# Optimization experiments

Hardware: AMD Instinct MI355X
Metric: run time of the kernel (lower is better)

The kernel has to match this reference:

```python
import jax, jax.numpy as jnp
import numpy as np

EPS = 1e-5
LOCAL_WINDOW = 256
NUM_HEADS = 16


def _layernorm(x, g, b):
    m = jnp.mean(x, axis=-1, keepdims=True)
    v = jnp.mean(jnp.square(x - m), axis=-1, keepdims=True)
    return (x - m) * jax.lax.rsqrt(v + EPS) * g + b


def _rotate_half(x):
    x1, x2 = jnp.split(x, 2, axis=-1)
    return jnp.concatenate([-x2, x1], axis=-1)


def _rope_cos_sin(s, d, base=10000.0):
    half = d // 2
    inv_freq = 1.0 / base ** (jnp.arange(half, dtype=jnp.float32) / float(half))
    t = jnp.arange(s, dtype=jnp.float32)
    freqs = jnp.einsum('s,d->sd', t, inv_freq)          # [s, half]
    emb = jnp.concatenate([freqs, freqs], axis=-1)       # [s, d]
    return jnp.cos(emb)[None, None, :, :], jnp.sin(emb)[None, None, :, :]


def setup_inputs() -> dict:
    key = jax.random.key(0)
    ks = jax.random.split(key, 8)
    B, S, D, F = 2, 2048, 1024, 4096
    sc = lambda d: 1.0 / np.sqrt(d)
    return {
        'x': jax.random.normal(ks[0], (B, S, D), jnp.float32),
        'w_qkv': jax.random.normal(ks[1], (D, 3 * D), jnp.float32) * sc(D),
        'w_out': jax.random.normal(ks[2], (D, D), jnp.float32) * sc(D),
        'g1': jnp.ones((D,), jnp.float32),
        'b1': jnp.zeros((D,), jnp.float32),
        'g2': jnp.ones((D,), jnp.float32),
        'b2': jnp.zeros((D,), jnp.float32),
        'w_gate': jax.random.normal(ks[3], (D, F), jnp.float32) * sc(D),
        'b_gate': jnp.zeros((F,), jnp.float32),
        'w_up': jax.random.normal(ks[4], (D, F), jnp.float32) * sc(D),
        'b_up': jnp.zeros((F,), jnp.float32),
        'w_down': jax.random.normal(ks[5], (F, D), jnp.float32) * sc(F),
        'b_down': jnp.zeros((D,), jnp.float32),
    }


def reference(x, w_qkv, w_out, g1, b1, g2, b2, w_gate, b_gate, w_up, b_up, w_down, b_down):
    B, S, D = x.shape
    H = NUM_HEADS
    hd = D // H

    # ---- pre-norm + RoPE self-attention ----
    y = _layernorm(x, g1, b1)
    qkv = jnp.einsum('bsd,de->bse', y, w_qkv)
    q, k, v = jnp.split(qkv, 3, axis=-1)
    split_heads = lambda t: t.reshape(B, S, H, hd).transpose(0, 2, 1, 3)  # [b,h,s,hd]
    q, k, v = split_heads(q), split_heads(k), split_heads(v)

    cos, sin = _rope_cos_sin(S, hd)
    q = q * cos + _rotate_half(q) * sin
    k = k * cos + _rotate_half(k) * sin

    scale = float(hd) ** -0.5
    logits = jnp.einsum('bhid,bhjd->bhij', q, k) * scale

    i = jnp.arange(S)[:, None]
    j = jnp.arange(S)[None, :]
    can = (jnp.abs(j - i) <= LOCAL_WINDOW) & (j <= i)    # local + causal band
    logits = jnp.where(can[None, None], logits, jnp.float32(-1e9))

    attn = jax.nn.softmax(logits, axis=-1)
    o = jnp.einsum('bhij,bhjd->bhid', attn, v)
    o = o.transpose(0, 2, 1, 3).reshape(B, S, D)
    x = x + jnp.einsum('bsd,de->bse', o, w_out)

    # ---- pre-norm + SwiGLU MLP ----
    y = _layernorm(x, g2, b2)
    gate = jnp.einsum('bsd,df->bsf', y, w_gate) + b_gate
    up = jnp.einsum('bsd,df->bsf', y, w_up) + b_up
    gated = gate * jax.nn.silu(up)
    x = x + jnp.einsum('bsf,fd->bsd', gated, w_down) + b_down
    return x
```

## Files before the change

### kernel.cpp

```cpp
#include <hip/hip_runtime.h>

typedef unsigned short u16;
typedef unsigned long long u64;
typedef __attribute__((ext_vector_type(8))) short bf16x8;
typedef __attribute__((ext_vector_type(4))) float f32x4;

__device__ inline u16 f2bf(float f) {
  unsigned int u = __float_as_uint(f);
  u += 0x7fffu + ((u >> 16) & 1u);
  return (u16)(u >> 16);
}
__device__ inline float bf2f(u16 h) { return __uint_as_float(((unsigned int)h) << 16); }

__device__ inline void gload_lds16(const void* gp, void* lp) {
  __builtin_amdgcn_global_load_lds(
      (const __attribute__((address_space(1))) unsigned int*)gp,
      (__attribute__((address_space(3))) unsigned int*)lp, 16, 0, 0);
}

__global__ __launch_bounds__(256) void ln_kernel(const float* __restrict__ x,
                                                 const float* __restrict__ g,
                                                 const float* __restrict__ beta,
                                                 u16* __restrict__ y) {
  __shared__ float red[8];
  const int row = blockIdx.x;
  const int t = threadIdx.x;
  const float4 xv = *(const float4*)(x + (long)row * 1024 + t * 4);
  float s = xv.x + xv.y + xv.z + xv.w;
  float sq = xv.x * xv.x + xv.y * xv.y + xv.z * xv.z + xv.w * xv.w;
#pragma unroll
  for (int d = 1; d < 64; d <<= 1) {
    s += __shfl_xor(s, d);
    sq += __shfl_xor(sq, d);
  }
  if ((t & 63) == 0) { red[t >> 6] = s; red[4 + (t >> 6)] = sq; }
  __syncthreads();
  s = red[0] + red[1] + red[2] + red[3];
  sq = red[4] + red[5] + red[6] + red[7];
  const float mean = s * (1.f / 1024.f);
  const float var = sq * (1.f / 1024.f) - mean * mean;
  const float inv = rsqrtf(var + 1e-5f);
  float xe[4] = {xv.x, xv.y, xv.z, xv.w};
  u16 ov[4];
#pragma unroll
  for (int e = 0; e < 4; ++e)
    ov[e] = f2bf((xe[e] - mean) * inv * g[t * 4 + e] + beta[t * 4 + e]);
  *(u64*)(y + (long)row * 1024 + t * 4) = *(u64*)ov;
}

__global__ __launch_bounds__(256) void transpose_bf16(const float* __restrict__ in,
                                                      u16* __restrict__ out,
                                                      int R, int C) {
  __shared__ float tile[64][33];
  const int t = threadIdx.x;
  const int tx = t & 31, ty = t >> 5;
  const int rx = t & 63, cy = t >> 6;
  const long r0 = (long)blockIdx.y * 64, c0 = (long)blockIdx.x * 32;
#pragma unroll
  for (int i = 0; i < 8; ++i)
    tile[ty + i * 8][tx] = in[(r0 + ty + i * 8) * C + c0 + tx];
  __syncthreads();
#pragma unroll
  for (int i = 0; i < 8; ++i)
    out[(c0 + i * 4 + cy) * R + r0 + rx] = f2bf(tile[rx][i * 4 + cy]);
}

__global__ __launch_bounds__(256) void transpose_ilv(const float* __restrict__ in,
                                                     u16* __restrict__ out,
                                                     int R, int C, int off) {
  __shared__ float tile[64][33];
  const int t = threadIdx.x;
  const int tx = t & 31, ty = t >> 5;
  const int rx = t & 63, cy = t >> 6;
  const long r0 = (long)blockIdx.y * 64, c0 = (long)blockIdx.x * 32;
#pragma unroll
  for (int i = 0; i < 8; ++i)
    tile[ty + i * 8][tx] = in[(r0 + ty + i * 8) * C + c0 + tx];
  __syncthreads();
#pragma unroll
  for (int i = 0; i < 8; ++i) {
    const int c = (int)c0 + i * 4 + cy;
    const long v = ((long)(c >> 4) << 5) + off + (c & 15);
    out[v * R + r0 + rx] = f2bf(tile[rx][i * 4 + cy]);
  }
}

__global__ __launch_bounds__(256) void trig_kernel(float* __restrict__ tbl) {
  const int i = blockIdx.x * 256 + threadIdx.x;
  const int s = i >> 5, d0 = i & 31;
  const float inv = exp2f((float)d0 * (-13.287712379549449f / 32.f));
  float sn, cs;
  sincosf((float)s * inv, &sn, &cs);
  tbl[i] = cs;
  tbl[65536 + i] = sn;
}

__global__ __launch_bounds__(64, 4) void attn_kernel(const u16* __restrict__ qr,
                                                     const u16* __restrict__ kr,
                                                     const u16* __restrict__ vt,
                                                     u16* __restrict__ o) {
  __shared__ __attribute__((aligned(16))) u16 Pl[16][40];
  int wg = blockIdx.x;
  wg = (wg & 7) * 512 + (wg >> 3);
  const int qt = wg & 127;
  const int bh = wg >> 7;
  const int qs = qt * 16;
  const int l = threadIdx.x;
  const int lr = l & 15, lg = l >> 4;
  const long bho = (long)(bh >> 4) * 2048 * 1024 + (long)(bh & 15) * 64;
  const long vtb = (long)bh * 64 * 2048;

  const u16* qp = qr + bho + (long)(qs + lr) * 1024 + lg * 8;
  const bf16x8 aq0 = *(const bf16x8*)qp;
  const bf16x8 aq1 = *(const bf16x8*)(qp + 32);

  f32x4 oacc[4];
#pragma unroll
  for (int nt = 0; nt < 4; ++nt) { oacc[nt][0] = 0.f; oacc[nt][1] = 0.f; oacc[nt][2] = 0.f; oacc[nt][3] = 0.f; }
  float m_[4], ls[4];
#pragma unroll
  for (int r = 0; r < 4; ++r) { m_[r] = -1e30f; ls[r] = 0.f; }

  for (int ch = 0; ch < 9; ++ch) {
    const int j0 = qs - 256 + ch * 32;
    if (j0 + 32 <= 0) continue;

    const int jc0u = j0 + lr;
    const int jc1u = j0 + 16 + lr;
    const int jc0 = min(max(jc0u, 0), 2047);
    const int jc1 = min(max(jc1u, 0), 2047);
    const u16* kp0 = kr + bho + (long)jc0 * 1024 + lg * 8;
    const u16* kp1 = kr + bho + (long)jc1 * 1024 + lg * 8;
    const bf16x8 b00 = *(const bf16x8*)kp0;
    const bf16x8 b01 = *(const bf16x8*)(kp0 + 32);
    const bf16x8 b10 = *(const bf16x8*)kp1;
    const bf16x8 b11 = *(const bf16x8*)(kp1 + 32);

    f32x4 z; z[0] = 0.f; z[1] = 0.f; z[2] = 0.f; z[3] = 0.f;
    f32x4 s0 = __builtin_amdgcn_mfma_f32_16x16x32_bf16(aq0, b00, z, 0, 0, 0);
    s0 = __builtin_amdgcn_mfma_f32_16x16x32_bf16(aq1, b01, s0, 0, 0, 0);
    f32x4 s1 = __builtin_amdgcn_mfma_f32_16x16x32_bf16(aq0, b10, z, 0, 0, 0);
    s1 = __builtin_amdgcn_mfma_f32_16x16x32_bf16(aq1, b11, s1, 0, 0, 0);

    float p0[4], p1[4], al[4];
#pragma unroll
    for (int r = 0; r < 4; ++r) {
      const int qg = qs + lg * 4 + r;
      const bool v0 = (jc0u >= 0) & (jc0u <= qg) & (qg - jc0u <= 256);
      const bool v1 = (jc1u >= 0) & (jc1u <= qg) & (qg - jc1u <= 256);
      const float t0 = v0 ? s0[r] : -1e30f;
      const float t1 = v1 ? s1[r] : -1e30f;
      float mx = fmaxf(t0, t1);
      mx = fmaxf(mx, __shfl_xor(mx, 1));
      mx = fmaxf(mx, __shfl_xor(mx, 2));
      mx = fmaxf(mx, __shfl_xor(mx, 4));
      mx = fmaxf(mx, __shfl_xor(mx, 8));
      const float mn = fmaxf(m_[r], mx);
      if (mn < -1e29f) {
        al[r] = 1.f; p0[r] = 0.f; p1[r] = 0.f;
      } else {
        al[r] = __expf(m_[r] - mn);
        p0[r] = (t0 < -1e29f) ? 0.f : __expf(t0 - mn);
        p1[r] = (t1 < -1e29f) ? 0.f : __expf(t1 - mn);
      }
      m_[r] = mn;
      float rs = p0[r] + p1[r];
      rs += __shfl_xor(rs, 1);
      rs += __shfl_xor(rs, 2);
      rs += __shfl_xor(rs, 4);
      rs += __shfl_xor(rs, 8);
      ls[r] = ls[r] * al[r] + rs;
    }
#pragma unroll
    for (int r = 0; r < 4; ++r) {
      Pl[lg * 4 + r][lr] = f2bf(p0[r]);
      Pl[lg * 4 + r][lr + 16] = f2bf(p1[r]);
    }
    asm volatile("s_waitcnt lgkmcnt(0)" ::: "memory");
    const bf16x8 pa = *(const bf16x8*)(&Pl[lr][lg * 8]);

    const int jb = min(max(j0 + lg * 8, 0), 2040);
    const u16* vp = vt + vtb + (long)lr * 2048 + jb;
#pragma unroll
    for (int nt = 0; nt < 4; ++nt) {
      const bf16x8 bv = *(const bf16x8*)(vp + (long)(nt * 16) * 2048);
      f32x4 oa = oacc[nt];
#pragma unroll
      for (int r = 0; r < 4; ++r) oa[r] *= al[r];
      oacc[nt] = __builtin_amdgcn_mfma_f32_16x16x32_bf16(pa, bv, oa, 0, 0, 0);
    }
  }
#pragma unroll
  for (int nt = 0; nt < 4; ++nt)
#pragma unroll
    for (int r = 0; r < 4; ++r) {
      const long qg = qs + lg * 4 + r;
      o[bho + qg * 1024 + nt * 16 + lr] = f2bf(oacc[nt][r] / ls[r]);
    }
}

__device__ __forceinline__ void stage_half(u16* lds, int ldsbase,
                                           const u16* gp, int ld, int col,
                                           int tid, int w) {
  const int r0 = tid >> 3;
  const int sw = ((tid & 7) ^ (r0 & 7)) << 3;
  gload_lds16(gp + (long)r0 * ld + col + sw, lds + ldsbase + w * 512);
  gload_lds16(gp + (long)(r0 + 64) * ld + col + sw, lds + ldsbase + 4096 + w * 512);
}

template <int EPI>
__global__ __launch_bounds__(512, 2) void gemm8p(const u16* __restrict__ A,
                                                 const u16* __restrict__ BT,
                                                 u16* __restrict__ Cb,
                                                 const float* __restrict__ bias,
                                                 float* __restrict__ Cf0,
                                                 float* __restrict__ Cf1,
                                                 u16* __restrict__ P1,
                                                 u16* __restrict__ P2,
                                                 const float* __restrict__ tbl,
                                                 int M, int N, int Kfull, int Kl) {
  __shared__ __attribute__((aligned(16))) u16 lds[81920];
  const int tid = threadIdx.x;
  const int w = tid >> 6, l = tid & 63;
  const int lr = l & 15, lg = l >> 4;
  const int l7 = l & 7;
  const int wr = w >> 2, wc = w & 3;
  const int nbx = N >> 8, nby = M >> 8;
  int wg = blockIdx.x;
  { const int cpx = gridDim.x >> 3; wg = (wg & 7) * cpx + (wg >> 3); }
  const int z = wg / (nbx * nby);
  const int rem = wg % (nbx * nby);
  const int rr = rem % (8 * nbx);
  const long m0 = (long)((rem / (8 * nbx)) * 8 + (rr & 7)) * 256;
  const long n0 = (long)(rr >> 3) * 256;
  const long koff = (long)z * Kl;
  const int NT = Kl >> 6;

  f32x4 acc[8][4];
#pragma unroll
  for (int i = 0; i < 8; ++i)
#pragma unroll
    for (int j = 0; j < 4; ++j) { acc[i][j][0] = 0.f; acc[i][j][1] = 0.f; acc[i][j][2] = 0.f; acc[i][j][3] = 0.f; }

  const u16* Alo = A + m0 * Kfull + koff;
  const u16* Ahi = A + (m0 + 128) * Kfull + koff;
  const u16* Blo = BT + n0 * Kfull + koff;
  const u16* Bhi = BT + (n0 + 128) * Kfull + koff;

  stage_half(lds, 0, Alo, Kfull, 0, tid, w);
  stage_half(lds, 8192, Ahi, Kfull, 0, tid, w);
  stage_half(lds, 49152, Blo, Kfull, 0, tid, w);
  stage_half(lds, 57344, Bhi, Kfull, 0, tid, w);
  stage_half(lds, 16384, Alo, Kfull, 64, tid, w);
  stage_half(lds, 24576, Ahi, Kfull, 64, tid, w);
  stage_half(lds, 65536, Blo, Kfull, 64, tid, w);
  stage_half(lds, 73728, Bhi, Kfull, 64, tid, w);
  asm volatile("s_waitcnt vmcnt(8)" ::: "memory");
  __builtin_amdgcn_s_barrier();

  for (int t = 0; t < NT; ++t) {
    const int abuf = t % 3;
    int sA = abuf + 2; if (sA >= 3) sA -= 3;
    const int p = t & 1;
    const int baA = abuf * 16384 + wr * 8192;
    const int bB = 49152 + p * 16384;
    bf16x8 b[4][2];
#pragma unroll
    for (int q = 0; q < 4; ++q) {
      bf16x8 a[2][2];
#pragma unroll
      for (int m2 = 0; m2 < 2; ++m2) {
        const int rowA = (q * 2 + m2) * 16 + lr;
#pragma unroll
        for (int kh = 0; kh < 2; ++kh)
          a[m2][kh] = *(const bf16x8*)(lds + baA + rowA * 64 + (((kh * 4 + lg) ^ l7) << 3));
      }
      if (q == 0) {
#pragma unroll
        for (int fn = 0; fn < 4; ++fn) {
          const int rb = wc * 64 + fn * 16 + lr;
#pragma unroll
          for (int kh = 0; kh < 2; ++kh)
            b[fn][kh] = *(const bf16x8*)(lds + bB + (rb >> 7) * 8192 + (rb & 127) * 64 + (((kh * 4 + lg) ^ l7) << 3));
        }
      }
      if (t + 2 < NT) {
        if (q == 0) stage_half(lds, sA * 16384, Alo, Kfull, (t + 2) * 64, tid, w);
        if (q == 1) stage_half(lds, sA * 16384 + 8192, Ahi, Kfull, (t + 2) * 64, tid, w);
        if (q == 2) stage_half(lds, bB, Blo, Kfull, (t + 2) * 64, tid, w);
        if (q == 3) stage_half(lds, bB + 8192, Bhi, Kfull, (t + 2) * 64, tid, w);
      }
      if (q == 0) { asm volatile("s_waitcnt lgkmcnt(8)" ::: "memory"); }

      __builtin_amdgcn_s_barrier();
      asm volatile("s_waitcnt lgkmcnt(0)" ::: "memory");
      __builtin_amdgcn_s_setprio(1);
#pragma unroll
      for (int m2 = 0; m2 < 2; ++m2)
#pragma unroll
        for (int fn = 0; fn < 4; ++fn)
#pragma unroll
          for (int kh = 0; kh < 2; ++kh)
            acc[q * 2 + m2][fn] = __builtin_amdgcn_mfma_f32_16x16x32_bf16(a[m2][kh], b[fn][kh], acc[q * 2 + m2][fn], 0, 0, 0);
      __builtin_amdgcn_s_setprio(0);
      if (q == 3) {
        if (t + 2 < NT) { asm volatile("s_waitcnt vmcnt(8)" ::: "memory"); }
        else            { asm volatile("s_waitcnt vmcnt(0)" ::: "memory"); }
      }
      __builtin_amdgcn_s_barrier();
    }
  }

  if constexpr (EPI == 6) {
    const int regn = (int)((n0 + wc * 64) >> 10);
    if (regn < 2) {
      const float scale = (regn == 0) ? 0.125f : 1.f;
      u16* dst = (regn == 0) ? Cb : P1;
      const int cbase = (int)(n0 & 1023) + wc * 64 + lr;
#pragma unroll
      for (int fm = 0; fm < 8; ++fm) {
        const long mr = m0 + wr * 128 + fm * 16 + lg * 4;
#pragma unroll
        for (int fn = 0; fn < 2; ++fn) {
          const int c1 = cbase + fn * 16;
          const int d0 = fn * 16 + lr;
#pragma unroll
          for (int r = 0; r < 4; ++r) {
            const long row = mr + r;
            const int s = (int)(row & 2047);
            const float cs = tbl[(s << 5) + d0];
            const float sn = tbl[65536 + (s << 5) + d0];
            const float x1v = acc[fm][fn][r], x2v = acc[fm][fn + 2][r];
            dst[row * 1024 + c1] = f2bf((x1v * cs - x2v * sn) * scale);
            dst[row * 1024 + c1 + 32] = f2bf((x2v * cs + x1v * sn) * scale);
          }
        }
      }
    } else {
#pragma unroll
      for (int fm = 0; fm < 8; ++fm) {
        const long mr = m0 + wr * 128 + fm * 16 + lg * 4;
        const int bb = (int)(mr >> 11);
        const int s = (int)(mr & 2047);
#pragma unroll
        for (int fn = 0; fn < 4; ++fn) {
          const int ncv = (int)(n0 - 2048) + wc * 64 + fn * 16 + lr;
          const int h = ncv >> 6, d = ncv & 63;
          u16 pk[4];
#pragma unroll
          for (int r = 0; r < 4; ++r) pk[r] = f2bf(acc[fm][fn][r]);
          *(u64*)(P2 + (long)(bb * 16 + h) * 131072 + (long)d * 2048 + s) = *(u64*)pk;
        }
      }
    }
    return;
  }

  if constexpr (EPI == 7) {
    const int rcb = (int)((n0 + wc * 64) >> 1);
#pragma unroll
    for (int fm = 0; fm < 8; ++fm) {
      const long mr = m0 + wr * 128 + fm * 16 + lg * 4;
#pragma unroll
      for (int fp = 0; fp < 2; ++fp) {
        const int rc = rcb + fp * 16 + lr;
        const float bg = bias[rc];
        const float bu = tbl[rc];
#pragma unroll
        for (int r = 0; r < 4; ++r) {
          const float g = acc[fm][2 * fp][r] + bg;
          const float u = acc[fm][2 * fp + 1][r] + bu;
          const float sg = 1.f / (1.f + __expf(-u));
          Cb[(mr + r) * 4096 + rc] = f2bf(g * u * sg);
        }
      }
    }
    return;
  }

  float* Cf = (z < 2 ? Cf0 : Cf1) + (long)(z & 1) * M * N;
#pragma unroll
  for (int fm = 0; fm < 8; ++fm) {
    const long mr = m0 + wr * 128 + fm * 16 + lg * 4;
#pragma unroll
    for (int fn = 0; fn < 4; ++fn) {
      const long nc = n0 + wc * 64 + fn * 16 + lr;
#pragma unroll
      for (int r = 0; r < 4; ++r)
        Cf[(mr + r) * N + nc] = acc[fm][fn][r];
    }
  }
}

__global__ __launch_bounds__(256) void combine_ln(const float* __restrict__ p0,
                                                  const float* __restrict__ p1,
                                                  const float* __restrict__ x,
                                                  const float* __restrict__ g,
                                                  const float* __restrict__ beta,
                                                  float* __restrict__ x1,
                                                  u16* __restrict__ y) {
  __shared__ float red[8];
  const long MN = (long)4096 * 1024;
  const int row = blockIdx.x;
  const int t = threadIdx.x;
  const long base = (long)row * 1024 + t * 4;
  const float4 a = *(const float4*)(p0 + base);
  const float4 b = *(const float4*)(p0 + MN + base);
  const float4 c = *(const float4*)(p1 + base);
  const float4 d = *(const float4*)(p1 + MN + base);
  const float4 r = *(const float4*)(x + base);
  float v[4] = {a.x + b.x + c.x + d.x + r.x, a.y + b.y + c.y + d.y + r.y,
                a.z + b.z + c.z + d.z + r.z, a.w + b.w + c.w + d.w + r.w};
  *(float4*)(x1 + base) = *(float4*)v;
  float s = v[0] + v[1] + v[2] + v[3];
  float sq = v[0] * v[0] + v[1] * v[1] + v[2] * v[2] + v[3] * v[3];
#pragma unroll
  for (int dd = 1; dd < 64; dd <<= 1) {
    s += __shfl_xor(s, dd);
    sq += __shfl_xor(sq, dd);
  }
  if ((t & 63) == 0) { red[t >> 6] = s; red[4 + (t >> 6)] = sq; }
  __syncthreads();
  s = red[0] + red[1] + red[2] + red[3];
  sq = red[4] + red[5] + red[6] + red[7];
  const float mean = s * (1.f / 1024.f);
  const float var = sq * (1.f / 1024.f) - mean * mean;
  const float inv = rsqrtf(var + 1e-5f);
  u16 ov[4];
#pragma unroll
  for (int e = 0; e < 4; ++e)
    ov[e] = f2bf((v[e] - mean) * inv * g[t * 4 + e] + beta[t * 4 + e]);
  *(u64*)(y + base) = *(u64*)ov;
}

__global__ __launch_bounds__(256) void combine4(const float* __restrict__ p0,
                                                const float* __restrict__ p1,
                                                const float* __restrict__ res,
                                                const float* __restrict__ bias,
                                                float* __restrict__ out) {
  const long MN = (long)4096 * 1024;
  const long i = ((long)blockIdx.x * 256 + threadIdx.x) * 4;
  const float4 a = *(const float4*)(p0 + i);
  const float4 b = *(const float4*)(p0 + MN + i);
  const float4 c = *(const float4*)(p1 + i);
  const float4 d = *(const float4*)(p1 + MN + i);
  const float4 r = *(const float4*)(res + i);
  const float4 bb = *(const float4*)(bias + (int)(i & 1023));
  float4 o;
  o.x = a.x + b.x + c.x + d.x + r.x + bb.x;
  o.y = a.y + b.y + c.y + d.y + r.y + bb.y;
  o.z = a.z + b.z + c.z + d.z + r.z + bb.z;
  o.w = a.w + b.w + c.w + d.w + r.w + bb.w;
  *(float4*)(out + i) = o;
}

extern "C" void kernel_launch(void* const* d_in, const int* in_sizes, int n_in,
                              void* d_out, int out_size, void* d_ws, size_t ws_size,
                              hipStream_t stream) {
  (void)in_sizes; (void)n_in; (void)out_size; (void)ws_size;
  const float* x      = (const float*)d_in[0];
  const float* w_qkv  = (const float*)d_in[1];
  const float* w_out  = (const float*)d_in[2];
  const float* g1     = (const float*)d_in[3];
  const float* b1     = (const float*)d_in[4];
  const float* g2     = (const float*)d_in[5];
  const float* b2     = (const float*)d_in[6];
  const float* w_gate = (const float*)d_in[7];
  const float* b_gate = (const float*)d_in[8];
  const float* w_up   = (const float*)d_in[9];
  const float* b_up   = (const float*)d_in[10];
  const float* w_down = (const float*)d_in[11];
  const float* b_down = (const float*)d_in[12];
  float* out = (float*)d_out;

  const size_t MB = 1u << 20;
  char* ws = (char*)d_ws;
  u16*   wdownT = (u16*)(ws + 0 * MB);
  u16*   y      = (u16*)(ws + 8 * MB);
  u16*   wqkvT  = (u16*)(ws + 16 * MB);
  u16*   woutT  = (u16*)(ws + 22 * MB);
  u16*   wguT   = (u16*)(ws + 24 * MB);
  u16*   qr_    = (u16*)(ws + 40 * MB);
  u16*   kr_    = (u16*)(ws + 48 * MB);
  u16*   vt     = (u16*)(ws + 56 * MB);
  float* trig   = (float*)(ws + 64 * MB);
  u16*   o_     = (u16*)(ws + 64 * MB);
  float* part0  = (float*)(ws + 72 * MB);
  float* part1  = (float*)(ws + 104 * MB);
  float* x1     = (float*)(ws + 56 * MB);
  u16*   gated  = (u16*)(ws + 104 * MB);
  float* pd0    = (float*)(ws + 16 * MB);
  float* pd1    = (float*)(ws + 72 * MB);

  const dim3 blk(256);
  transpose_bf16<<<dim3(3072 / 32, 1024 / 64), blk, 0, stream>>>(w_qkv, wqkvT, 1024, 3072);
  transpose_bf16<<<dim3(1024 / 32, 1024 / 64), blk, 0, stream>>>(w_out, woutT, 1024, 1024);
  transpose_ilv<<<dim3(4096 / 32, 1024 / 64), blk, 0, stream>>>(w_gate, wguT, 1024, 4096, 0);
  transpose_ilv<<<dim3(4096 / 32, 1024 / 64), blk, 0, stream>>>(w_up, wguT, 1024, 4096, 16);
  transpose_bf16<<<dim3(1024 / 32, 4096 / 64), blk, 0, stream>>>(w_down, wdownT, 4096, 1024);
  trig_kernel<<<256, blk, 0, stream>>>(trig);

  ln_kernel<<<4096, blk, 0, stream>>>(x, g1, b1, y);
  gemm8p<6><<<dim3((3072 / 256) * (4096 / 256)), dim3(512), 0, stream>>>(
      y, wqkvT, qr_, nullptr, nullptr, nullptr, kr_, vt, trig,
      4096, 3072, 1024, 1024);
  attn_kernel<<<4096, dim3(64), 0, stream>>>(qr_, kr_, vt, o_);
  gemm8p<0><<<dim3(4 * 16 * 4), dim3(512), 0, stream>>>(
      o_, woutT, nullptr, nullptr, part0, part1, nullptr, nullptr, nullptr,
      4096, 1024, 1024, 256);
  combine_ln<<<4096, blk, 0, stream>>>(part0, part1, x, g2, b2, x1, y);
  gemm8p<7><<<dim3((8192 / 256) * (4096 / 256)), dim3(512), 0, stream>>>(
      y, wguT, gated, b_gate, nullptr, nullptr, nullptr, nullptr, b_up,
      4096, 8192, 1024, 1024);
  gemm8p<0><<<dim3(4 * 16 * 4), dim3(512), 0, stream>>>(
      gated, wdownT, nullptr, nullptr, pd0, pd1, nullptr, nullptr, nullptr,
      4096, 1024, 4096, 1024);
  combine4<<<4096, blk, 0, stream>>>(pd0, pd1, x1, b_down, out);
}
```

Baseline: 273.1 us.

## Replace split-K partial buffers with atomic accumulation and double-buffer A fragments

The split-K GEMMs (attention output projection and MLP down projection) now accumulate straight into a pre-filled residual buffer with float atomics, instead of writing four partial fp32 slabs and reducing them in combine kernels. The residual is seeded by a device memcpy and a small bias-add kernel, and the second layernorm reuses the plain ln_kernel. Separately, the GEMM main loop double-buffers A fragments in registers, loads B once per k-step, and drops one barrier and its lgkmcnt waits per sub-step. This removes a lot of partial-sum memory traffic, at the cost of atomic contention, non-deterministic summation order, and possible LDS hazards from the removed barrier.

Measured after the change: 328.5 us. 1.2x slower.

```diff
diff --git a/kernel.cpp b/kernel.cpp
--- a/kernel.cpp
+++ b/kernel.cpp
@@ -93,6 +93,16 @@
   sincosf((float)s * inv, &sn, &cs);
   tbl[i] = cs;
   tbl[65536 + i] = sn;
+}
+
+__global__ __launch_bounds__(256) void prefill_add(const float* __restrict__ x1,
+                                                   const float* __restrict__ bias,
+                                                   float* __restrict__ out) {
+  const long i = ((long)blockIdx.x * 256 + threadIdx.x) * 4;
+  float4 v = *(const float4*)(x1 + i);
+  const float4 bb = *(const float4*)(bias + (int)(i & 1023));
+  v.x += bb.x; v.y += bb.y; v.z += bb.z; v.w += bb.w;
+  *(float4*)(out + i) = v;
 }
 
 __global__ __launch_bounds__(64, 4) void attn_kernel(const u16* __restrict__ qr,
@@ -214,7 +224,6 @@
                                                  u16* __restrict__ Cb,
                                                  const float* __restrict__ bias,
                                                  float* __restrict__ Cf0,
-                                                 float* __restrict__ Cf1,
                                                  u16* __restrict__ P1,
                                                  u16* __restrict__ P2,
                                                  const float* __restrict__ tbl,
@@ -264,36 +273,27 @@
     const int p = t & 1;
     const int baA = abuf * 16384 + wr * 8192;
     const int bB = 49152 + p * 16384;
-    bf16x8 b[4][2];
+    bf16x8 aA[2][2], aB[2][2], b[4][2];
+#pragma unroll
+    for (int m2 = 0; m2 < 2; ++m2)
+#pragma unroll
+      for (int kh = 0; kh < 2; ++kh)
+        aA[m2][kh] = *(const bf16x8*)(lds + baA + (m2 * 16 + lr) * 64 + (((kh * 4 + lg) ^ l7) << 3));
+#pragma unroll
+    for (int fn = 0; fn < 4; ++fn) {
+      const int rb = wc * 64 + fn * 16 + lr;
+#pragma unroll
+      for (int kh = 0; kh < 2; ++kh)
+        b[fn][kh] = *(const bf16x8*)(lds + bB + (rb >> 7) * 8192 + (rb & 127) * 64 + (((kh * 4 + lg) ^ l7) << 3));
+    }
 #pragma unroll
     for (int q = 0; q < 4; ++q) {
-      bf16x8 a[2][2];
-#pragma unroll
-      for (int m2 = 0; m2 < 2; ++m2) {
-        const int rowA = (q * 2 + m2) * 16 + lr;
-#pragma unroll
-        for (int kh = 0; kh < 2; ++kh)
-          a[m2][kh] = *(const bf16x8*)(lds + baA + rowA * 64 + (((kh * 4 + lg) ^ l7) << 3));
-      }
-      if (q == 0) {
-#pragma unroll
-        for (int fn = 0; fn < 4; ++fn) {
-          const int rb = wc * 64 + fn * 16 + lr;
-#pragma unroll
-          for (int kh = 0; kh < 2; ++kh)
-            b[fn][kh] = *(const bf16x8*)(lds + bB + (rb >> 7) * 8192 + (rb & 127) * 64 + (((kh * 4 + lg) ^ l7) << 3));
-        }
-      }
       if (t + 2 < NT) {
         if (q == 0) stage_half(lds, sA * 16384, Alo, Kfull, (t + 2) * 64, tid, w);
         if (q == 1) stage_half(lds, sA * 16384 + 8192, Ahi, Kfull, (t + 2) * 64, tid, w);
         if (q == 2) stage_half(lds, bB, Blo, Kfull, (t + 2) * 64, tid, w);
         if (q == 3) stage_half(lds, bB + 8192, Bhi, Kfull, (t + 2) * 64, tid, w);
       }
-      if (q == 0) { asm volatile("s_waitcnt lgkmcnt(8)" ::: "memory"); }
-
-      __builtin_amdgcn_s_barrier();
-      asm volatile("s_waitcnt lgkmcnt(0)" ::: "memory");
       __builtin_amdgcn_s_setprio(1);
 #pragma unroll
       for (int m2 = 0; m2 < 2; ++m2)
@@ -301,8 +301,19 @@
         for (int fn = 0; fn < 4; ++fn)
 #pragma unroll
           for (int kh = 0; kh < 2; ++kh)
-            acc[q * 2 + m2][fn] = __builtin_amdgcn_mfma_f32_16x16x32_bf16(a[m2][kh], b[fn][kh], acc[q * 2 + m2][fn], 0, 0, 0);
+            acc[q * 2 + m2][fn] = __builtin_amdgcn_mfma_f32_16x16x32_bf16(
+                (q & 1) ? aB[m2][kh] : aA[m2][kh], b[fn][kh], acc[q * 2 + m2][fn], 0, 0, 0);
       __builtin_amdgcn_s_setprio(0);
+      if (q < 3) {
+#pragma unroll
+        for (int m2 = 0; m2 < 2; ++m2)
+#pragma unroll
+          for (int kh = 0; kh < 2; ++kh) {
+            const int rowA = ((q + 1) * 2 + m2) * 16 + lr;
+            const bf16x8 v = *(const bf16x8*)(lds + baA + rowA * 64 + (((kh * 4 + lg) ^ l7) << 3));
+            if (q & 1) aA[m2][kh] = v; else aB[m2][kh] = v;
+          }
+      }
       if (q == 3) {
         if (t + 2 < NT) { asm volatile("s_waitcnt vmcnt(8)" ::: "memory"); }
         else            { asm volatile("s_waitcnt vmcnt(0)" ::: "memory"); }
@@ -378,80 +389,20 @@
     return;
   }
 
-  float* Cf = (z < 2 ? Cf0 : Cf1) + (long)(z & 1) * M * N;
-#pragma unroll
-  for (int fm = 0; fm < 8; ++fm) {
-    const long mr = m0 + wr * 128 + fm * 16 + lg * 4;
-#pragma unroll
-    for (int fn = 0; fn < 4; ++fn) {
-      const long nc = n0 + wc * 64 + fn * 16 + lr;
-#pragma unroll
-      for (int r = 0; r < 4; ++r)
-        Cf[(mr + r) * N + nc] = acc[fm][fn][r];
-    }
-  }
-}
-
-__global__ __launch_bounds__(256) void combine_ln(const float* __restrict__ p0,
-                                                  const float* __restrict__ p1,
-                                                  const float* __restrict__ x,
-                                                  const float* __restrict__ g,
-                                                  const float* __restrict__ beta,
-                                                  float* __restrict__ x1,
-                                                  u16* __restrict__ y) {
-  __shared__ float red[8];
-  const long MN = (long)4096 * 1024;
-  const int row = blockIdx.x;
-  const int t = threadIdx.x;
-  const long base = (long)row * 1024 + t * 4;
-  const float4 a = *(const float4*)(p0 + base);
-  const float4 b = *(const float4*)(p0 + MN + base);
-  const float4 c = *(const float4*)(p1 + base);
-  const float4 d = *(const float4*)(p1 + MN + base);
-  const float4 r = *(const float4*)(x + base);
-  float v[4] = {a.x + b.x + c.x + d.x + r.x, a.y + b.y + c.y + d.y + r.y,
-                a.z + b.z + c.z + d.z + r.z, a.w + b.w + c.w + d.w + r.w};
-  *(float4*)(x1 + base) = *(float4*)v;
-  float s = v[0] + v[1] + v[2] + v[3];
-  float sq = v[0] * v[0] + v[1] * v[1] + v[2] * v[2] + v[3] * v[3];
-#pragma unroll
-  for (int dd = 1; dd < 64; dd <<= 1) {
-    s += __shfl_xor(s, dd);
-    sq += __shfl_xor(sq, dd);
-  }
-  if ((t & 63) == 0) { red[t >> 6] = s; red[4 + (t >> 6)] = sq; }
-  __syncthreads();
-  s = red[0] + red[1] + red[2] + red[3];
-  sq = red[4] + red[5] + red[6] + red[7];
-  const float mean = s * (1.f / 1024.f);
-  const float var = sq * (1.f / 1024.f) - mean * mean;
-  const float inv = rsqrtf(var + 1e-5f);
-  u16 ov[4];
-#pragma unroll
-  for (int e = 0; e < 4; ++e)
-    ov[e] = f2bf((v[e] - mean) * inv * g[t * 4 + e] + beta[t * 4 + e]);
-  *(u64*)(y + base) = *(u64*)ov;
-}
-
-__global__ __launch_bounds__(256) void combine4(const float* __restrict__ p0,
-                                                const float* __restrict__ p1,
-                                                const float* __restrict__ res,
-                                                const float* __restrict__ bias,
-                                                float* __restrict__ out) {
-  const long MN = (long)4096 * 1024;
-  const long i = ((long)blockIdx.x * 256 + threadIdx.x) * 4;
-  const float4 a = *(const float4*)(p0 + i);
-  const float4 b = *(const float4*)(p0 + MN + i);
-  const float4 c = *(const float4*)(p1 + i);
-  const float4 d = *(const float4*)(p1 + MN + i);
-  const float4 r = *(const float4*)(res + i);
-  const float4 bb = *(const float4*)(bias + (int)(i & 1023));
-  float4 o;
-  o.x = a.x + b.x + c.x + d.x + r.x + bb.x;
-  o.y = a.y + b.y + c.y + d.y + r.y + bb.y;
-  o.z = a.z + b.z + c.z + d.z + r.z + bb.z;
-  o.w = a.w + b.w + c.w + d.w + r.w + bb.w;
-  *(float4*)(out + i) = o;
+  if constexpr (EPI == 8) {
+#pragma unroll
+    for (int fm = 0; fm < 8; ++fm) {
+      const long mr = m0 + wr * 128 + fm * 16 + lg * 4;
+#pragma unroll
+      for (int fn = 0; fn < 4; ++fn) {
+        const long nc = n0 + wc * 64 + fn * 16 + lr;
+#pragma unroll
+        for (int r = 0; r < 4; ++r)
+          unsafeAtomicAdd(&Cf0[(mr + r) * N + nc], acc[fm][fn][r]);
+      }
+    }
+    return;
+  }
 }
 
 extern "C" void kernel_launch(void* const* d_in, const int* in_sizes, int n_in,
@@ -485,12 +436,8 @@
   u16*   vt     = (u16*)(ws + 56 * MB);
   float* trig   = (float*)(ws + 64 * MB);
   u16*   o_     = (u16*)(ws + 64 * MB);
-  float* part0  = (float*)(ws + 72 * MB);
-  float* part1  = (float*)(ws + 104 * MB);
-  float* x1     = (float*)(ws + 56 * MB);
-  u16*   gated  = (u16*)(ws + 104 * MB);
-  float* pd0    = (float*)(ws + 16 * MB);
-  float* pd1    = (float*)(ws + 72 * MB);
+  float* x1     = (float*)(ws + 72 * MB);
+  u16*   gated  = (u16*)(ws + 88 * MB);
 
   const dim3 blk(256);
   transpose_bf16<<<dim3(3072 / 32, 1024 / 64), blk, 0, stream>>>(w_qkv, wqkvT, 1024, 3072);
@@ -502,18 +449,18 @@
 
   ln_kernel<<<4096, blk, 0, stream>>>(x, g1, b1, y);
   gemm8p<6><<<dim3((3072 / 256) * (4096 / 256)), dim3(512), 0, stream>>>(
-      y, wqkvT, qr_, nullptr, nullptr, nullptr, kr_, vt, trig,
-      4096, 3072, 1024, 1024);
+      y, wqkvT, qr_, nullptr, nullptr, kr_, vt, trig, 4096, 3072, 1024, 1024);
   attn_kernel<<<4096, dim3(64), 0, stream>>>(qr_, kr_, vt, o_);
-  gemm8p<0><<<dim3(4 * 16 * 4), dim3(512), 0, stream>>>(
-      o_, woutT, nullptr, nullptr, part0, part1, nullptr, nullptr, nullptr,
+  hipMemcpyAsync(x1, x, (size_t)4096 * 1024 * 4, hipMemcpyDeviceToDevice, stream);
+  gemm8p<8><<<dim3(4 * 16 * 4), dim3(512), 0, stream>>>(
+      o_, woutT, nullptr, nullptr, x1, nullptr, nullptr, nullptr,
       4096, 1024, 1024, 256);
-  combine_ln<<<4096, blk, 0, stream>>>(part0, part1, x, g2, b2, x1, y);
+  ln_kernel<<<4096, blk, 0, stream>>>(x1, g2, b2, y);
   gemm8p<7><<<dim3((8192 / 256) * (4096 / 256)), dim3(512), 0, stream>>>(
-      y, wguT, gated, b_gate, nullptr, nullptr, nullptr, nullptr, b_up,
+      y, wguT, gated, b_gate, nullptr, nullptr, nullptr, b_up,
       4096, 8192, 1024, 1024);
-  gemm8p<0><<<dim3(4 * 16 * 4), dim3(512), 0, stream>>>(
-      gated, wdownT, nullptr, nullptr, pd0, pd1, nullptr, nullptr, nullptr,
+  prefill_add<<<4096, blk, 0, stream>>>(x1, b_down, out);
+  gemm8p<8><<<dim3(4 * 16 * 4), dim3(512), 0, stream>>>(
+      gated, wdownT, nullptr, nullptr, out, nullptr, nullptr, nullptr,
       4096, 1024, 4096, 1024);
-  combine4<<<4096, blk, 0, stream>>>(pd0, pd1, x1, b_down, out);
-}
+}
```
